# Optimization experiments

Measured on AMD Instinct MI355X. Metric: run time of the kernel, lower is better.

Reference implementation:

```python
import jax, jax.numpy as jnp
import numpy as np

EPS_D = 1e-12  # clamp for sqrt of pairwise distances (diag is exactly 0)


def tr2dist_small(Y):
    # Y: (B, k, N) -> (B, N, N); standard protein-folding coords->distance map
    k = Y.shape[1]
    Z = Y - jnp.mean(Y, axis=2, keepdims=True)
    n2 = jnp.sum(Z * Z, axis=1)                        # (B, N)
    D = n2[:, None, :] + n2[:, :, None] - 2.0 * jnp.einsum('bkn,bkm->bnm', Z, Z)
    D = 3.0 * D / k
    return jnp.sqrt(jnp.maximum(D, EPS_D))


def mean_masked(X, mask, axis, keepdims=True):
    return jnp.sum(X * mask, axis=axis, keepdims=keepdims) / jnp.sum(mask, axis=axis, keepdims=keepdims)


def get_graph_lap(X, mask):
    # X: (B, C, N), mask: (B, 1, N)
    B, C, N = X.shape
    mm = jnp.einsum('bin,bim->bnm', mask, mask)        # (B, N, N) pair mask
    X = X - mean_masked(X, mask, axis=2) * mask
    X = X / jnp.sqrt(jnp.sum(X * X, axis=2, keepdims=True) / jnp.sum(mask, axis=2, keepdims=True) + 1e-4)
    pos = 0.5 * jnp.linspace(0.0, 1.0, N)[None, :] * mask   # (B, 1, N)
    Xa = jnp.concatenate((X, pos), axis=1)
    Wd = tr2dist_small(Xa) * mm
    sigma = mean_masked(Wd, mm, axis=(1, 2))           # (B, 1, 1)
    Wd = jnp.exp(-Wd / sigma * 10.0) * mm
    Wsum = jnp.sum(Wd, axis=1)                         # (B, N)
    L = jnp.zeros_like(Wd) + Wsum[:, :, None] * jnp.eye(N, dtype=Wd.dtype)[None] - Wd
    L = 0.5 * (L + jnp.swapaxes(L, 1, 2))
    return L, Wd


def _forward(Z, mask, K0, Knet, W, Wend):
    h = 0.01
    m = mask[:, None, :]                               # (B, 1, N)
    Z = jnp.tanh(jnp.einsum('oc,bcn->bon', K0, Z)) * m
    nlayers = W.shape[0]
    for i in range(nlayers):
        L, _ = get_graph_lap(Z, m)
        Ki = Knet[i]
        Wi = W[i, :, :, :, 0]                          # (3, C, C) size-1 kernels
        cv = lambda w, x: jnp.einsum('oc,bcn->bon', w, x) * m     # conv1d, k=1
        cvT = lambda w, x: jnp.einsum('co,bcn->bon', w, x) * m    # conv_transpose1d, k=1
        mm1 = lambda x: jnp.einsum('bcn,bnm->bcm', x, L)
        Ai = Ki[0] * cv(Wi[0], Z) + mm1(Ki[1] * cv(Wi[1], Z)) + mm1(mm1(Ki[2] * cv(Wi[2], Z)))
        Ai = (Ai - mean_masked(Ai, m, axis=2)) * m
        Ai = Ai / jnp.sqrt(jnp.sum(Ai * Ai, axis=1, keepdims=True) + 0.001)
        Ai = jax.nn.relu(Ai)
        Ai = Ki[0] * cvT(Wi[0], Ai) + mm1(Ki[1] * cvT(Wi[1], Ai)) + mm1(mm1(Ki[2] * cvT(Wi[2], Ai)))
        Z = Z - h * Ai
    Zout = jnp.einsum('oc,bcn->bon', Wend[:, :, 0], Z) * m       # (B, chan_out, N)
    dists = tuple(tr2dist_small(Zout[:, 3 * i:3 * i + 3, :]) for i in range(Zout.shape[1] // 3))
    return dists + (Zout,)


def setup_inputs() -> dict:
    key = jax.random.key(0)
    ks = jax.random.split(key, 6)
    B, chan_in, chan_out, channels, N, nlayers = 16, 40, 3, 256, 1024, 6
    stdv0 = 0.1 * channels / chan_in
    return {
        'Z': jax.random.normal(ks[0], (B, chan_in, N), dtype=jnp.float32),
        'mask': jnp.ones((B, N), dtype=jnp.float32),
        'K0': jax.random.uniform(ks[1], (channels, chan_in), minval=-stdv0, maxval=stdv0, dtype=jnp.float32),
        'Knet': jax.random.uniform(ks[2], (nlayers, chan_out), minval=-stdv0, maxval=stdv0, dtype=jnp.float32),
        'W': jax.random.uniform(ks[3], (nlayers, 3, channels, channels, 1), minval=-0.1, maxval=0.1, dtype=jnp.float32),
        'Wend': 1e-4 * jax.random.normal(ks[4], (chan_out, channels, 1), dtype=jnp.float32),
    }


def reference(Z, mask, K0, Knet, W, Wend):
    return _forward(Z, mask, K0, Knet, W, Wend)
```

## Files before the change

kernel.cpp:

```cpp
#include <hip/hip_runtime.h>
#include <hip/hip_fp16.h>
#include <math.h>

#define BB 16
#define CIN 40
#define CH 256
#define NN 1024
#define KROWS 257
#define KPAD 288
#define NLAYERS 6

typedef unsigned short ush;
typedef __attribute__((ext_vector_type(8))) short bh8;
typedef __attribute__((ext_vector_type(8))) _Float16 h8;
typedef __attribute__((ext_vector_type(4))) float f4;

__device__ __forceinline__ ush bf16_rne(float x) {
  unsigned int u = __float_as_uint(x);
  u += 0x7fffu + ((u >> 16) & 1u);
  return (ush)(u >> 16);
}
__device__ __forceinline__ float bf16_f(ush h) {
  return __uint_as_float(((unsigned int)h) << 16);
}
// ... 181 lines not shown
  s1 = blockReduceSum(s1);
  s2 = blockReduceSum(s2);
  if (threadIdx.x == 0) {
    const size_t base = ((size_t)b * CH + o) * 8;
    statS1[base] = s1; statS2[base] = s2;
    #pragma unroll
    for (int k = 1; k < 8; k++) { statS1[base + k] = 0.f; statS2[base + k] = 0.f; }
  }
}

__global__ void masksum_kernel(const float* __restrict__ mask, float* __restrict__ msum,
                               float* __restrict__ pmpos) {
  const int b = blockIdx.x;
  float v = 0.f, p = 0.f;
  for (int n = threadIdx.x; n < NN; n += 256) {
    const float m = mask[b * NN + n];
    v += m;
    p += 0.5f * ((float)n * (1.0f / (NN - 1))) * m;
  }
  v = blockReduceSum(v);
  p = blockReduceSum(p);
  if (threadIdx.x == 0) { msum[b] = v; pmpos[b] = p * (1.0f / NN); }
}

__global__ void wprep_kernel(const float* __restrict__ W, ush* __restrict__ Wm,
                             ush* __restrict__ Wt) {
  __shared__ float t[64][65];
  const int mat = blockIdx.y;
  const int ty = blockIdx.x >> 2, tx = blockIdx.x & 3;
  const float* src = W + (size_t)mat * CH * CH;
  const int tid = threadIdx.x;
  const int lr = tid >> 2;
  const int lc = (tid & 3) * 16;
  float v[16];
  #pragma unroll
  for (int j = 0; j < 16; j += 4)
    *(float4*)&v[j] = *(const float4*)&src[(size_t)(ty * 64 + lr) * CH + tx * 64 + lc + j];
  ush hv[16];
  #pragma unroll
  for (int j = 0; j < 16; j++) {
    hv[j] = f2h(v[j]);
    t[lr][lc + j] = v[j];
  }
  const size_t offm = (size_t)mat * CH * CH + (size_t)(ty * 64 + lr) * CH + tx * 64 + lc;
  #pragma unroll
  for (int j = 0; j < 16; j += 4)
    *(ushort4*)&Wm[offm + j] = *(ushort4*)&hv[j];
  __syncthreads();
  #pragma unroll
  for (int j = 0; j < 16; j++) hv[j] = f2h(t[lc + j][lr]);
  const size_t offt = (size_t)mat * CH * CH + (size_t)(tx * 64 + lr) * CH + ty * 64 + lc;
  #pragma unroll
  for (int j = 0; j < 16; j += 4)
    *(ushort4*)&Wt[offt + j] = *(ushort4*)&hv[j];
}

__global__ void rowstatZ_kernel(const float* __restrict__ statS1, const float* __restrict__ statS2,
                                const float* __restrict__ msum, float* __restrict__ muZ,
                                float* __restrict__ rsZ) {
  const int b = blockIdx.x;
  const int c = threadIdx.x;
  const size_t base = ((size_t)b * CH + c) * 8;
  float S1 = 0.f, S2 = 0.f;
  #pragma unroll
  for (int k = 0; k < 8; k++) { S1 += statS1[base + k]; S2 += statS2[base + k]; }
  const float M = msum[b];
  const float mu = S1 / M;
  const float q = fmaxf(S2 - mu * S1, 0.f);
  muZ[b * CH + c] = mu;
  rsZ[b * CH + c] = 1.0f / sqrtf(q / M + 1e-4f);
}

__global__ void rowstatU_kernel(const float* __restrict__ statS1, const float* __restrict__ msum,
                                float* __restrict__ rmean) {
  const int b = blockIdx.x;
  const int c = threadIdx.x;
  const size_t base = ((size_t)b * CH + c) * 8;
  float S1 = 0.f;
  #pragma unroll
  for (int k = 0; k < 8; k++) S1 += statS1[base + k];
  rmean[b * CH + c] = S1 / msum[b];
}

__global__ void tsplitY_kernel(const float* __restrict__ Zcur, const float* __restrict__ mask,
                               const float* __restrict__ muZ, const float* __restrict__ rsZ,
                               const float* __restrict__ pmpos, ush* __restrict__ Th,
                               ush* __restrict__ Tl, float* __restrict__ n2part) {
  __shared__ float t[32][65];
  const int b = blockIdx.z;
  const int n0 = blockIdx.x * 64;
  const int k0 = blockIdx.y * 32;
  const int tid = threadIdx.x;
  const int lr = tid >> 3;
  const int lc = (tid & 7) * 8;
  const int gk = k0 + lr;
  float xv[8];
  if (gk < CH) {
    const float mu = muZ[b * CH + gk];
    const float rs = rsZ[b * CH + gk];
    const float* zr = Zcur + ((size_t)b * CH + gk) * NN + n0 + lc;
    const float* mr = mask + b * NN + n0 + lc;
    const float4 z0 = *(const float4*)&zr[0];
    const float4 z1 = *(const float4*)&zr[4];
    const float4 m0 = *(const float4*)&mr[0];
    const float4 m1 = *(const float4*)&mr[4];
    xv[0] = (z0.x - mu * m0.x) * rs; xv[1] = (z0.y - mu * m0.y) * rs;
    xv[2] = (z0.z - mu * m0.z) * rs; xv[3] = (z0.w - mu * m0.w) * rs;
    xv[4] = (z1.x - mu * m1.x) * rs; xv[5] = (z1.y - mu * m1.y) * rs;
    xv[6] = (z1.z - mu * m1.z) * rs; xv[7] = (z1.w - mu * m1.w) * rs;
  } else if (gk == CH) {
    const float pm = pmpos[b];
    #pragma unroll
    for (int j = 0; j < 8; j++) {
      const int n = n0 + lc + j;
      xv[j] = 0.5f * ((float)n * (1.0f / (NN - 1))) * mask[b * NN + n] - pm;
    }
  } else {
    #pragma unroll
    for (int j = 0; j < 8; j++) xv[j] = 0.f;
  }
  #pragma unroll
  for (int j = 0; j < 8; j++) t[lr][lc + j] = xv[j];
  __syncthreads();
  const int on = tid >> 2;
  const int ok = (tid & 3) * 8;
  ush hv[8], lv[8];
  float s = 0.f;
  #pragma unroll
  for (int j = 0; j < 8; j++) {
    const float v = t[ok + j][on];
    s += v * v;
    hv[j] = bf16_rne(v); lv[j] = bf16_rne(v - bf16_f(hv[j]));
  }
  const size_t off = ((size_t)b * NN + n0 + on) * KPAD + k0 + ok;
  *(ushort4*)&Th[off] = *(ushort4*)&hv[0];
  *(ushort4*)&Th[off + 4] = *(ushort4*)&hv[4];
  *(ushort4*)&Tl[off] = *(ushort4*)&lv[0];
  *(ushort4*)&Tl[off + 4] = *(ushort4*)&lv[4];
  s += __shfl_xor(s, 1, 64);
  s += __shfl_xor(s, 2, 64);
  if ((tid & 3) == 0) n2part[((size_t)b * 9 + blockIdx.y) * NN + n0 + on] = s;
}

__global__ void n2red_kernel(const float* __restrict__ n2part, float* __restrict__ n2) {
  const int idx = blockIdx.x * 256 + threadIdx.x;
  const int b = idx >> 10, n = idx & 1023;
  float s = 0.f;
  #pragma unroll
  for (int kb = 0; kb < 9; kb++) s += n2part[((size_t)b * 9 + kb) * NN + n];
  n2[idx] = s;
}

__global__ __launch_bounds__(256, 2)
void gram_v4_kernel(const ush* __restrict__ Yth, const ush* __restrict__ Ytl,
                    const float* __restrict__ n2, const float* __restrict__ mask,
                    ush* __restrict__ Dp, float* __restrict__ sigpart) {
  __shared__ ush lds[32768];
  const int bid = blockIdx.x;
  const int logical = (bid & 7) * 72 + (bid >> 3);
  const int b = logical / 36;
  int t = logical - b * 36;
  int ty = 0;
  while (t >= 8 - ty) { t -= 8 - ty; ++ty; }
  const int tx = ty + t;
  const int i0 = ty * 128;
  const int j0 = tx * 128;
  const ush* Ah = Yth + (size_t)b * NN * KPAD + (size_t)i0 * KPAD;
  const ush* Al = Ytl + (size_t)b * NN * KPAD + (size_t)i0 * KPAD;
  const ush* Bh = Yth + (size_t)b * NN * KPAD + (size_t)j0 * KPAD;
  const ush* Bl = Ytl + (size_t)b * NN * KPAD + (size_t)j0 * KPAD;
  f4 acc[4][4];
  const f4 z4 = {0.f, 0.f, 0.f, 0.f};
  #pragma unroll
  for (int mi = 0; mi < 4; mi++)
    #pragma unroll
    for (int ni = 0; ni < 4; ni++) acc[mi][ni] = z4;
  stageA(Ah, Al, KPAD, Bh, Bl, KPAD, 0, lds);
  __syncthreads();
  int pb = 0;
  for (int kt = 32; kt < KPAD; kt += 32) {
    stageA(Ah, Al, KPAD, Bh, Bl, KPAD, kt, lds + (pb ^ 1) * 16384);
    computeA(lds + pb * 16384, acc);
    __syncthreads();
    pb ^= 1;
  }
  computeA(lds + pb * 16384, acc);
  const int lane = threadIdx.x & 63;
  const int wid = threadIdx.x >> 6;
  const int wr = wid >> 1, wc = wid & 1;
  const int frow = lane & 15, hh = lane >> 4;
  const float scale = 3.0f / 257.0f;
  float lsum = 0.f;
  #pragma unroll
  for (int ni = 0; ni < 4; ni++) {
    const int jl = wc * 64 + ni * 16 + frow;
    const int j = j0 + jl;
    const float n2j = n2[b * NN + j];
    const float mkj = mask[b * NN + j];
    #pragma unroll
    for (int mi = 0; mi < 4; mi++) {
      const int il = wr * 64 + mi * 16 + hh * 4;
      ush dv[4];
      #pragma unroll
      for (int r = 0; r < 4; r++) {
        const int i = i0 + il + r;
        const float D = scale * (n2[b * NN + i] + n2j - 2.0f * acc[mi][ni][r]);
        const float d = sqrtf(fmaxf(D, 1e-12f));
        const float mmv = mask[b * NN + i] * mkj;
        const float wd = d * mmv;
        lsum += wd * mmv;
        dv[r] = f2h(wd);
      }
      if (ty != tx) {
        uint2 mr;
        mr.x = (unsigned)dv[0] | ((unsigned)dv[1] << 16);
        mr.y = (unsigned)dv[2] | ((unsigned)dv[3] << 16);
        *(uint2*)&Dp[((size_t)b * NN + j) * NN + i0 + il] = mr;
      }
      #pragma unroll
      for (int r = 0; r < 4; r++) {
        const unsigned v = dv[r];
        const unsigned vp = (unsigned)__shfl_xor((int)v, 1, 64);
        if ((frow & 1) == 0)
          *(unsigned*)&Dp[((size_t)b * NN + i0 + il + r) * NN + j] = v | (vp << 16);
      }
    }
  }
  if (ty != tx) lsum *= 2.0f;
  #pragma unroll
  for (int off = 32; off > 0; off >>= 1) lsum += __shfl_down(lsum, off, 64);
  __syncthreads();
  float* rbuf = (float*)lds;
  if (lane == 0) rbuf[wid] = lsum;
  __syncthreads();
  if (threadIdx.x == 0)
    sigpart[(size_t)b * 64 + ty * 8 + tx] = rbuf[0] + rbuf[1] + rbuf[2] + rbuf[3];
}

__global__ void sigfinal_kernel(const float* __restrict__ sigpart, const float* __restrict__ msum,
                                float* __restrict__ fbuf) {
  const int b = blockIdx.x;
  float v = 0.f;
  if (threadIdx.x < 64) {
    const int ty = threadIdx.x >> 3, tx = threadIdx.x & 7;
    if (ty <= tx) v = sigpart[b * 64 + threadIdx.x];
  }
  v = blockReduceSum(v);
  if (threadIdx.x == 0) { const float ms = msum[b]; fbuf[b] = -10.0f * ms * ms / v; }
}

__global__ void expw3_kernel(const ush* __restrict__ Dp, const float* __restrict__ mask,
                             const float* __restrict__ fbuf, ush* __restrict__ Wp) {
  const int b = blockIdx.y, n = blockIdx.x;
  const float fb = fbuf[b];
  const float mn = mask[b * NN + n];
  const size_t roff = ((size_t)b * NN + n) * NN;
  const int t = threadIdx.x;
  const float4 mk = ((const float4*)(mask + b * NN))[t];
  const ushort4 dp = *(const ushort4*)&Dp[roff + t * 4];
  const float w0 = expf(fb * h2f(dp.x)) * mn * mk.x;
  const float w1 = expf(fb * h2f(dp.y)) * mn * mk.y;
  const float w2 = expf(fb * h2f(dp.z)) * mn * mk.z;
  const float w3 = expf(fb * h2f(dp.w)) * mn * mk.w;
  const float s = blockReduceSum(w0 + w1 + w2 + w3);
  float v0 = -w0, v1 = -w1, v2 = -w2, v3 = -w3;
  if ((n >> 2) == t) {
    const int r = n & 3;
    if (r == 0) v0 += s; else if (r == 1) v1 += s; else if (r == 2) v2 += s; else v3 += s;
  }
  ushort4 h4;
  h4.x = f2h(v0); h4.y = f2h(v1); h4.z = f2h(v2); h4.w = f2h(v3);
  *(ushort4*)&Wp[roff + t * 4] = h4;
}

__global__ void tsplitZ_kernel(const float* __restrict__ in, ush* __restrict__ Th,
                               ush* __restrict__ Tl) {
  __shared__ float t[32][65];
  const int b = blockIdx.z;
  const int n0 = blockIdx.x * 64;
  const int k0 = blockIdx.y * 32;
  const float* src = in + (size_t)b * CH * NN;
  const int tid = threadIdx.x;
  const int lr = tid >> 3;
  const int lc = (tid & 7) * 8;
  const int gk = k0 + lr;
  *(float4*)&t[lr][lc]     = *(const float4*)&src[(size_t)gk * NN + n0 + lc];
  *(float4*)&t[lr][lc + 4] = *(const float4*)&src[(size_t)gk * NN + n0 + lc + 4];
  __syncthreads();
  const int on = tid >> 2;
  const int ok = (tid & 3) * 8;
  ush hv[8], lv[8];
  #pragma unroll
  for (int j = 0; j < 8; j++) {
    const float v = t[ok + j][on];
    hv[j] = f2h(v); lv[j] = f2h(v - h2f(hv[j]));
  }
  const size_t off = ((size_t)b * NN + n0 + on) * CH + k0 + ok;
  *(ushort4*)&Th[off] = *(ushort4*)&hv[0];
  *(ushort4*)&Th[off + 4] = *(ushort4*)&hv[4];
  *(ushort4*)&Tl[off] = *(ushort4*)&lv[0];
  *(ushort4*)&Tl[off + 4] = *(ushort4*)&lv[4];
}

__global__ __launch_bounds__(256, 2)
void cvall_kernel(const ush* __restrict__ Ap, const ush* __restrict__ Bth,
                  const ush* __restrict__ Btl, const float* __restrict__ mask,
                  const float* __restrict__ Kis, unsigned int* __restrict__ Cpack,
                  ush* __restrict__ C2h, ush* __restrict__ C2l) {
  __shared__ ush lds[32768];
  const int bid = blockIdx.x;
  const int logical = (bid & 7) * 96 + (bid >> 3);
  const int b = logical / 48;
  const int inner = logical - b * 48;
  const int c0g = inner & 7;
  const int r0g = inner >> 3;
  const int r0 = r0g * 128;
  const int c0 = c0g * 128;
  const ush* Aq = Ap + (size_t)r0 * CH;
  const ush* Bh = Bth + (size_t)b * NN * CH + (size_t)c0 * CH;
  const ush* Bl = Btl + (size_t)b * NN * CH + (size_t)c0 * CH;
  f4 acc[4][4];
  const f4 z4 = {0.f, 0.f, 0.f, 0.f};
  #pragma unroll
  for (int mi = 0; mi < 4; mi++)
    #pragma unroll
    for (int ni = 0; ni < 4; ni++) acc[mi][ni] = z4;
  stageCV(Aq, CH, Bh, Bl, CH, 0, lds);
  __syncthreads();
  int pb = 0;
  for (int kt = 32; kt < CH; kt += 32) {
    stageCV(Aq, CH, Bh, Bl, CH, kt, lds + (pb ^ 1) * 12288);
    computeCV(lds + pb * 12288, acc);
    __syncthreads();
    pb ^= 1;
  }
  computeCV(lds + pb * 12288, acc);
  __syncthreads();
  unsigned int* tl = (unsigned int*)lds;
  const int lane = threadIdx.x & 63;
  const int wid = threadIdx.x >> 6;
  const int wr = wid >> 1, wc = wid & 1;
  const int frow = lane & 15, hh = lane >> 4;
  const float alpha = Kis[r0g >> 1];
  #pragma unroll
  for (int ni = 0; ni < 4; ni++) {
    const int jl = wc * 64 + ni * 16 + frow;
    const float am = alpha * mask[b * NN + c0 + jl];
    #pragma unroll
    for (int mi = 0; mi < 4; mi++) {
      const int il = wr * 64 + mi * 16 + hh * 4;
      unsigned int pv[4];
      #pragma unroll
      for (int r = 0; r < 4; r++) {
        const float v = acc[mi][ni][r] * am;
        const ush h = f2h(v);
        const ush l = f2h(v - h2f(h));
        pv[r] = (unsigned int)h | ((unsigned int)l << 16);
      }
      const int slot = (il >> 2) ^ (jl & 31);
      *(uint4*)&tl[jl * 128 + slot * 4] = *(uint4*)pv;
    }
  }
  __syncthreads();
  const int rrow = threadIdx.x >> 1;
  const int rch = (threadIdx.x & 1) * 64;
  if (r0g < 4) {
    unsigned int* dst = Cpack + ((size_t)b * 512 + r0 + rrow) * NN + c0 + rch;
    #pragma unroll
    for (int g = 0; g < 16; g++) {
      unsigned int pw[4];
      #pragma unroll
      for (int q = 0; q < 4; q++) {
        const int jl = rch + g * 4 + q;
        const int slot = (rrow >> 2) ^ (jl & 31);
        pw[q] = tl[jl * 128 + slot * 4 + (rrow & 3)];
      }
      *(uint4*)&dst[g * 4] = *(uint4*)pw;
    }
  } else {
    const size_t obase = ((size_t)b * 256 + (r0 - 512) + rrow) * NN + c0 + rch;
    #pragma unroll
    for (int g = 0; g < 8; g++) {
      unsigned int hw[4], lw[4];
      #pragma unroll
      for (int q = 0; q < 4; q++) {
        unsigned int h2[2], l2[2];
        #pragma unroll
        for (int e = 0; e < 2; e++) {
          const int jl = rch + g * 8 + q * 2 + e;
          const int slot = (rrow >> 2) ^ (jl & 31);
          const unsigned int v = tl[jl * 128 + slot * 4 + (rrow & 3)];
          h2[e] = v & 0xffffu; l2[e] = v >> 16;
        }
        hw[q] = h2[0] | (h2[1] << 16);
        lw[q] = l2[0] | (l2[1] << 16);
      }
      *(uint4*)&C2h[obase + g * 8] = *(uint4*)hw;
      *(uint4*)&C2l[obase + g * 8] = *(uint4*)lw;
    }
  }
}

template <int OUTMODE, int STATS>
__global__ __launch_bounds__(256, 3)
void mm1_v5_kernel(const ush* __restrict__ Xh, const ush* __restrict__ Xl, const size_t xStride,
                   const ush* __restrict__ Wp,
                   const unsigned int* __restrict__ addp, const size_t aStride,
                   const float* __restrict__ zin, const float* __restrict__ mask,
                   float* __restrict__ outF, ush* __restrict__ outH, ush* __restrict__ outL,
                   float* __restrict__ statS1, float* __restrict__ statS2) {
  __shared__ ush lds[16384];
  const int bid = blockIdx.x;
  const int logical = (bid & 7) * 64 + (bid >> 3);
  const int b = logical >> 5;
  const int inner = logical & 31;
  const int n0 = (inner & 7) * 128;
  const int r0 = (inner >> 3) * 64;
  const ush* Ah = Xh + (size_t)b * xStride + (size_t)r0 * NN;
  const ush* Al = Xl + (size_t)b * xStride + (size_t)r0 * NN;
  const ush* Bp = Wp + (size_t)b * NN * NN + (size_t)n0 * NN;
  f4 acc[4][2];
  const f4 z4 = {0.f, 0.f, 0.f, 0.f};
  #pragma unroll
  for (int mi = 0; mi < 4; mi++) { acc[mi][0] = z4; acc[mi][1] = z4; }
  stageMM(Ah, Al, NN, Bp, NN, 0, lds);
  __syncthreads();
  int pb = 0;
  for (int kt = 32; kt < NN; kt += 32) {
    stageMM(Ah, Al, NN, Bp, NN, kt, lds + (pb ^ 1) * 8192);
    computeMM(lds + pb * 8192, acc);
    __syncthreads();
    pb ^= 1;
  }
  computeMM(lds + pb * 8192, acc);
  const int lane = threadIdx.x & 63;
  const int wid = threadIdx.x >> 6;
  const int frow = lane & 15, hh = lane >> 4;
  if (OUTMODE == 0) {
    __syncthreads();
    unsigned int* tl = (unsigned int*)lds;
    #pragma unroll
    for (int ni = 0; ni < 2; ni++) {
      const int jl = wid * 32 + ni * 16 + frow;
      const int col = n0 + jl;
      #pragma unroll
      for (int mi = 0; mi < 4; mi++) {
        const int il = mi * 16 + hh * 4;
        unsigned int pv[4];
        #pragma unroll
        for (int r = 0; r < 4; r++) {
          const int row = r0 + il + r;
          const unsigned int av = addp[(size_t)b * aStride + (size_t)row * NN + col];
          const float o = acc[mi][ni][r] + h2f((ush)(av & 0xffffu)) + h2f((ush)(av >> 16));
          const ush h = f2h(o);
          const ush l = f2h(o - h2f(h));
          pv[r] = (unsigned int)h | ((unsigned int)l << 16);
        }
        const int slot = (il >> 2) ^ (jl & 15);
        *(uint4*)&tl[jl * 64 + slot * 4] = *(uint4*)pv;
      }
    }
    __syncthreads();
    const int rrow = threadIdx.x >> 2;
    const int rch = (threadIdx.x & 3) * 32;
    const size_t obase = ((size_t)b * 256 + r0 + rrow) * NN + n0 + rch;
    #pragma unroll
    for (int g = 0; g < 4; g++) {
      unsigned int hw[4], lw[4];
      #pragma unroll
      for (int q = 0; q < 4; q++) {
        unsigned int h2[2], l2[2];
        #pragma unroll
        for (int e = 0; e < 2; e++) {
          const int jl = rch + g * 8 + q * 2 + e;
          const int slot = (rrow >> 2) ^ (jl & 15);
          const unsigned int v = tl[jl * 64 + slot * 4 + (rrow & 3)];
          h2[e] = v & 0xffffu; l2[e] = v >> 16;
        }
        hw[q] = h2[0] | (h2[1] << 16);
        lw[q] = l2[0] | (l2[1] << 16);
      }
      *(uint4*)&outH[obase + g * 8] = *(uint4*)hw;
      *(uint4*)&outL[obase + g * 8] = *(uint4*)lw;
    }
  } else {
    float a1[4][4];
    float a2[4][4];
    if (STATS) {
      #pragma unroll
      for (int mi = 0; mi < 4; mi++)
        #pragma unroll
        for (int r = 0; r < 4; r++) { a1[mi][r] = 0.f; a2[mi][r] = 0.f; }
    }
    #pragma unroll
    for (int ni = 0; ni < 2; ni++) {
      const int col = n0 + wid * 32 + ni * 16 + frow;
      const float mk = STATS ? mask[b * NN + col] : 0.f;
      #pragma unroll
      for (int mi = 0; mi < 4; mi++) {
        #pragma unroll
        for (int r = 0; r < 4; r++) {
          const int row = r0 + mi * 16 + hh * 4 + r;
          const unsigned int av = addp[(size_t)b * aStride + (size_t)row * NN + col];
          const float o = acc[mi][ni][r] + h2f((ush)(av & 0xffffu)) + h2f((ush)(av >> 16));
          const size_t ooff = (size_t)b * CH * NN + (size_t)row * NN + col;
          float val;
          if (OUTMODE == 1) val = o;
          else val = zin[ooff] - 0.01f * o;
          outF[ooff] = val;
          if (STATS) { a1[mi][r] += val * mk; a2[mi][r] += val * val * mk; }
        }
      }
    }
    if (STATS) {
      #pragma unroll
      for (int mi = 0; mi < 4; mi++)
        #pragma unroll
        for (int r = 0; r < 4; r++) {
          #pragma unroll
          for (int d = 1; d < 16; d <<= 1) {
            a1[mi][r] += __shfl_xor(a1[mi][r], d, 64);
            a2[mi][r] += __shfl_xor(a2[mi][r], d, 64);
          }
        }
      __syncthreads();
      float* s1b = (float*)lds;
      float* s2b = s1b + 256;
      if (frow == 0) {
        #pragma unroll
        for (int mi = 0; mi < 4; mi++)
          #pragma unroll
          for (int r = 0; r < 4; r++) {
            const int row = mi * 16 + hh * 4 + r;
            s1b[wid * 64 + row] = a1[mi][r];
            s2b[wid * 64 + row] = a2[mi][r];
          }
      }
      __syncthreads();
      if (threadIdx.x < 64) {
        const int row = threadIdx.x;
        const float p1 = s1b[row] + s1b[64 + row] + s1b[128 + row] + s1b[192 + row];
        const float p2 = s2b[row] + s2b[64 + row] + s2b[128 + row] + s2b[192 + row];
        const int nblk = n0 >> 7;
        statS1[((size_t)b * CH + r0 + row) * 8 + nblk] = p1;
        statS2[((size_t)b * CH + r0 + row) * 8 + nblk] = p2;
      }
    }
  }
}

__global__ void csq_kernel(const float* __restrict__ U, const float* __restrict__ mask,
                           const float* __restrict__ rmean, float* __restrict__ part) {
  const int b = blockIdx.y, cc = blockIdx.x;
  const int n = threadIdx.x * 4;
  const float4 m4 = *(const float4*)&mask[b * NN + n];
  float4 s4 = {0.f, 0.f, 0.f, 0.f};
  for (int r = 0; r < 16; r++) {
    const int c = cc * 16 + r;
    const float rm = rmean[b * CH + c];
    const float4 u4 = *(const float4*)&U[((size_t)b * CH + c) * NN + n];
    float a;
    a = (u4.x - rm) * m4.x; s4.x += a * a;
    a = (u4.y - rm) * m4.y; s4.y += a * a;
    a = (u4.z - rm) * m4.z; s4.z += a * a;
    a = (u4.w - rm) * m4.w; s4.w += a * a;
  }
  *(float4*)&part[((size_t)(b * 16 + cc)) * NN + n] = s4;
}

__global__ void csq2_kernel(const float* __restrict__ part, float* __restrict__ rs) {
  const int b = blockIdx.y;
  const int n = blockIdx.x * 256 + threadIdx.x;
  float s = 0.001f;
  #pragma unroll
  for (int cc = 0; cc < 16; cc++) s += part[((size_t)(b * 16 + cc)) * NN + n];
  rs[b * NN + n] = 1.0f / sqrtf(s);
}

__global__ void tsplitN_kernel(const float* __restrict__ U, const float* __restrict__ mask,
                               const float* __restrict__ rmean, const float* __restrict__ rs,
                               ush* __restrict__ Th, ush* __restrict__ Tl) {
  __shared__ float t[32][65];
  const int b = blockIdx.z;
  const int n0 = blockIdx.x * 64;
  const int k0 = blockIdx.y * 32;
  const int tid = threadIdx.x;
  const int lr = tid >> 3;
  const int lc = (tid & 7) * 8;
  const int gc = k0 + lr;
  const float rm = rmean[b * CH + gc];
  const float4 ma = *(const float4*)&mask[b * NN + n0 + lc];
  const float4 mb = *(const float4*)&mask[b * NN + n0 + lc + 4];
  const float4 ra = *(const float4*)&rs[b * NN + n0 + lc];
  const float4 rb = *(const float4*)&rs[b * NN + n0 + lc + 4];
  const float4 ua = *(const float4*)&U[((size_t)b * CH + gc) * NN + n0 + lc];
  const float4 ub = *(const float4*)&U[((size_t)b * CH + gc) * NN + n0 + lc + 4];
  t[lr][lc + 0] = fmaxf((ua.x - rm) * ma.x * ra.x, 0.f);
  t[lr][lc + 1] = fmaxf((ua.y - rm) * ma.y * ra.y, 0.f);
  t[lr][lc + 2] = fmaxf((ua.z - rm) * ma.z * ra.z, 0.f);
  t[lr][lc + 3] = fmaxf((ua.w - rm) * ma.w * ra.w, 0.f);
  t[lr][lc + 4] = fmaxf((ub.x - rm) * mb.x * rb.x, 0.f);
  t[lr][lc + 5] = fmaxf((ub.y - rm) * mb.y * rb.y, 0.f);
  t[lr][lc + 6] = fmaxf((ub.z - rm) * mb.z * rb.z, 0.f);
  t[lr][lc + 7] = fmaxf((ub.w - rm) * mb.w * rb.w, 0.f);
  __syncthreads();
  const int on = tid >> 2;
  const int ok = (tid & 3) * 8;
  ush hv[8], lv[8];
  #pragma unroll
  for (int j = 0; j < 8; j++) {
    const float v = t[ok + j][on];
    hv[j] = f2h(v); lv[j] = f2h(v - h2f(hv[j]));
  }
  const size_t off = ((size_t)b * NN + n0 + on) * CH + k0 + ok;
  *(ushort4*)&Th[off] = *(ushort4*)&hv[0];
  *(ushort4*)&Th[off + 4] = *(ushort4*)&hv[4];
  *(ushort4*)&Tl[off] = *(ushort4*)&lv[0];
  *(ushort4*)&Tl[off + 4] = *(ushort4*)&lv[4];
}

__global__ void zout_kernel(const float* __restrict__ Z, const float* __restrict__ Wend,
                            const float* __restrict__ mask, float* __restrict__ outZ,
                            float* __restrict__ Zcent) {
  const int b = blockIdx.x;
  __shared__ float w[3 * CH];
  for (int i = threadIdx.x; i < 3 * CH; i += 256) w[i] = Wend[i];
  __syncthreads();
  float a[3][4];
  #pragma unroll
  for (int j = 0; j < 4; j++) { a[0][j] = 0.f; a[1][j] = 0.f; a[2][j] = 0.f; }
  const float* Zb = Z + (size_t)b * CH * NN;
  for (int c = 0; c < CH; c++) {
    const float w0 = w[c], w1 = w[CH + c], w2 = w[2 * CH + c];
    #pragma unroll
    for (int j = 0; j < 4; j++) {
      float zv = Zb[(size_t)c * NN + threadIdx.x + j * 256];
      a[0][j] += w0 * zv; a[1][j] += w1 * zv; a[2][j] += w2 * zv;
    }
  }
  float sum[3] = {0.f, 0.f, 0.f};
  #pragma unroll
  for (int j = 0; j < 4; j++) {
    const int n = threadIdx.x + j * 256;
    const float mv = mask[b * NN + n];
    #pragma unroll
    for (int o = 0; o < 3; o++) {
      a[o][j] *= mv;
      outZ[((size_t)b * 3 + o) * NN + n] = a[o][j];
      sum[o] += a[o][j];
    }
  }
  for (int o = 0; o < 3; o++) {
    float s = blockReduceSum(sum[o]);
    const float mean = s * (1.0f / NN);
    #pragma unroll
    for (int j = 0; j < 4; j++) {
      const int n = threadIdx.x + j * 256;
      Zcent[((size_t)b * 3 + o) * NN + n] = a[o][j] - mean;
    }
  }
}

__global__ void dist_kernel(const float* __restrict__ Zcent, float* __restrict__ outD) {
  const int b = blockIdx.z;
  const int n = blockIdx.y;
  const int m = blockIdx.x * 256 + threadIdx.x;
  const float* Zb = Zcent + (size_t)b * 3 * NN;
  const float x0 = Zb[n], x1 = Zb[NN + n], x2 = Zb[2 * NN + n];
  const float d0 = x0 - Zb[m], d1 = x1 - Zb[NN + m], d2 = x2 - Zb[2 * NN + m];
  const float D = d0 * d0 + d1 * d1 + d2 * d2;
  outD[((size_t)b * NN + n) * NN + m] = sqrtf(fmaxf(D, 1e-12f));
}

extern "C" void kernel_launch(void* const* d_in, const int* in_sizes, int n_in,
                              void* d_out, int out_size, void* d_ws, size_t ws_size,
                              hipStream_t stream) {
  const float* Zin  = (const float*)d_in[0];
  const float* mask = (const float*)d_in[1];
  const float* K0   = (const float*)d_in[2];
  const float* Knet = (const float*)d_in[3];
  const float* W    = (const float*)d_in[4];
  const float* Wend = (const float*)d_in[5];
  float* out = (float*)d_out;

  ush* Wp = (ush*)out;
  ush* Dp = Wp + (size_t)BB * NN * NN;
  float* outZ = out + (size_t)BB * NN * NN;

  float* p = (float*)d_ws;
  float* uni = p; p += (size_t)BB * 768 * NN;
  ush* Yth = (ush*)uni;
  ush* Ytl = Yth + (size_t)BB * NN * KPAD;
  unsigned int* Cpack = (unsigned int*)uni;
  ush* C2h = (ush*)(uni + (size_t)BB * 512 * NN);
  ush* C2l = C2h + (size_t)BB * 256 * NN;

  float* Zcur = p; p += (size_t)BB * CH * NN;
  float* U    = p; p += (size_t)BB * CH * NN;
  ush* Zth = (ush*)p; p += (size_t)BB * NN * CH / 2;
  ush* Ztl = (ush*)p; p += (size_t)BB * NN * CH / 2;
  ush* Thb = Zth;
  ush* Tlb = Ztl;
  ush* Wm = (ush*)p; p += (size_t)18 * CH * CH / 2;
  ush* Wt = (ush*)p; p += (size_t)18 * CH * CH / 2;
  float* n2b   = p; p += BB * NN;
  float* rsb   = p; p += BB * NN;
  float* msum  = p; p += BB;
  float* pmpos = p; p += BB;
  float* sigp  = p; p += BB * 64;
  float* fbuf  = p; p += BB;
  float* rmeanb= p; p += BB * CH;
  float* muZ   = p; p += BB * CH;
  float* rsZ   = p; p += BB * CH;
  float* statS1= p; p += (size_t)BB * CH * 8;
  float* statS2= p; p += (size_t)BB * CH * 8;
  float* n2part= p; p += (size_t)BB * 9 * NN;
  float* partb = p; p += (size_t)BB * 16 * NN;
  float* Zcent = p; p += BB * 3 * NN;

  const dim3 gtsZ(NN / 64, CH / 32, BB);
  const dim3 gtsY(NN / 64, KPAD / 32, BB);
  const size_t sC = (size_t)512 * NN;
  const size_t sT = (size_t)CH * NN;

  masksum_kernel<<<BB, 256, 0, stream>>>(mask, msum, pmpos);
  wprep_kernel<<<dim3(16, 18), 256, 0, stream>>>(W, Wm, Wt);
  k0_kernel<<<dim3(CH, BB), 256, 0, stream>>>(Zin, K0, mask, Zcur, statS1, statS2);

  for (int layer = 0; layer < NLAYERS; layer++) {
    rowstatZ_kernel<<<BB, 256, 0, stream>>>(statS1, statS2, msum, muZ, rsZ);
    tsplitY_kernel<<<gtsY, 256, 0, stream>>>(Zcur, mask, muZ, rsZ, pmpos, Yth, Ytl, n2part);
    n2red_kernel<<<BB * NN / 256, 256, 0, stream>>>(n2part, n2b);
    gram_v4_kernel<<<576, 256, 0, stream>>>(Yth, Ytl, n2b, mask, Dp, sigp);
    sigfinal_kernel<<<BB, 256, 0, stream>>>(sigp, msum, fbuf);
    expw3_kernel<<<dim3(NN, BB), 256, 0, stream>>>(Dp, mask, fbuf, Wp);
    tsplitZ_kernel<<<gtsZ, 256, 0, stream>>>(Zcur, Zth, Ztl);

    const ush* Am = Wm + (size_t)layer * 3 * CH * CH;
    const ush* At = Wt + (size_t)layer * 3 * CH * CH;
    const float* Ki = Knet + layer * 3;

    cvall_kernel<<<768, 256, 0, stream>>>(Am, Zth, Ztl, mask, Ki, Cpack, C2h, C2l);
    mm1_v5_kernel<0, 0><<<512, 256, 0, stream>>>(C2h, C2l, sT, Wp,
        Cpack + (size_t)256 * NN, sC, nullptr, nullptr, nullptr, Thb, Tlb, nullptr, nullptr);
    mm1_v5_kernel<1, 1><<<512, 256, 0, stream>>>(Thb, Tlb, sT, Wp,
        Cpack, sC, nullptr, mask, U, nullptr, nullptr, statS1, statS2);

    rowstatU_kernel<<<BB, 256, 0, stream>>>(statS1, msum, rmeanb);
    csq_kernel<<<dim3(16, BB), 256, 0, stream>>>(U, mask, rmeanb, partb);
    csq2_kernel<<<dim3(NN / 256, BB), 256, 0, stream>>>(partb, rsb);
    tsplitN_kernel<<<gtsZ, 256, 0, stream>>>(U, mask, rmeanb, rsb, Zth, Ztl);

    cvall_kernel<<<768, 256, 0, stream>>>(At, Zth, Ztl, mask, Ki, Cpack, C2h, C2l);
    mm1_v5_kernel<0, 0><<<512, 256, 0, stream>>>(C2h, C2l, sT, Wp,
        Cpack + (size_t)256 * NN, sC, nullptr, nullptr, nullptr, Thb, Tlb, nullptr, nullptr);
    mm1_v5_kernel<2, 1><<<512, 256, 0, stream>>>(Thb, Tlb, sT, Wp,
        Cpack, sC, Zcur, mask, Zcur, nullptr, nullptr, statS1, statS2);
  }

  zout_kernel<<<BB, 256, 0, stream>>>(Zcur, Wend, mask, outZ, Zcent);
  dist_kernel<<<dim3(NN / 256, NN, BB), 256, 0, stream>>>(Zcent, out);
}
```

Measured before the change: 1.801 ms.

## Emit fp16 hi/lo split Z and U from mm1 epilogue, drop separate transposes

```diff
diff --git a/kernel.cpp b/kernel.cpp
--- a/kernel.cpp
+++ b/kernel.cpp
@@ -287,64 +287,89 @@
   rmean[b * CH + c] = S1 / msum[b];
 }
 
-__global__ void tsplitY_kernel(const float* __restrict__ Zcur, const float* __restrict__ mask,
-                               const float* __restrict__ muZ, const float* __restrict__ rsZ,
-                               const float* __restrict__ pmpos, ush* __restrict__ Th,
-                               ush* __restrict__ Tl, float* __restrict__ n2part) {
+__global__ void tsplitZ_kernel(const float* __restrict__ in, ush* __restrict__ Th,
+                               ush* __restrict__ Tl) {
   __shared__ float t[32][65];
   const int b = blockIdx.z;
   const int n0 = blockIdx.x * 64;
   const int k0 = blockIdx.y * 32;
+  const float* src = in + (size_t)b * CH * NN;
   const int tid = threadIdx.x;
   const int lr = tid >> 3;
   const int lc = (tid & 7) * 8;
   const int gk = k0 + lr;
-  float xv[8];
-  if (gk < CH) {
-    const float mu = muZ[b * CH + gk];
-    const float rs = rsZ[b * CH + gk];
-    const float* zr = Zcur + ((size_t)b * CH + gk) * NN + n0 + lc;
-    const float* mr = mask + b * NN + n0 + lc;
-    const float4 z0 = *(const float4*)&zr[0];
-    const float4 z1 = *(const float4*)&zr[4];
-    const float4 m0 = *(const float4*)&mr[0];
-    const float4 m1 = *(const float4*)&mr[4];
-    xv[0] = (z0.x - mu * m0.x) * rs; xv[1] = (z0.y - mu * m0.y) * rs;
-    xv[2] = (z0.z - mu * m0.z) * rs; xv[3] = (z0.w - mu * m0.w) * rs;
-    xv[4] = (z1.x - mu * m1.x) * rs; xv[5] = (z1.y - mu * m1.y) * rs;
-    xv[6] = (z1.z - mu * m1.z) * rs; xv[7] = (z1.w - mu * m1.w) * rs;
-  } else if (gk == CH) {
-    const float pm = pmpos[b];
-    #pragma unroll
-    for (int j = 0; j < 8; j++) {
-      const int n = n0 + lc + j;
-      xv[j] = 0.5f * ((float)n * (1.0f / (NN - 1))) * mask[b * NN + n] - pm;
-    }
-  } else {
-    #pragma unroll
-    for (int j = 0; j < 8; j++) xv[j] = 0.f;
-  }
-  #pragma unroll
-  for (int j = 0; j < 8; j++) t[lr][lc + j] = xv[j];
+  *(float4*)&t[lr][lc]     = *(const float4*)&src[(size_t)gk * NN + n0 + lc];
+  *(float4*)&t[lr][lc + 4] = *(const float4*)&src[(size_t)gk * NN + n0 + lc + 4];
   __syncthreads();
   const int on = tid >> 2;
   const int ok = (tid & 3) * 8;
   ush hv[8], lv[8];
-  float s = 0.f;
   #pragma unroll
   for (int j = 0; j < 8; j++) {
     const float v = t[ok + j][on];
-    s += v * v;
-    hv[j] = bf16_rne(v); lv[j] = bf16_rne(v - bf16_f(hv[j]));
-  }
-  const size_t off = ((size_t)b * NN + n0 + on) * KPAD + k0 + ok;
+    hv[j] = f2h(v); lv[j] = f2h(v - h2f(hv[j]));
+  }
+  const size_t off = ((size_t)b * NN + n0 + on) * CH + k0 + ok;
+  *(ushort4*)&Th[off] = *(ushort4*)&hv[0];
+  *(ushort4*)&Th[off + 4] = *(ushort4*)&hv[4];
+  *(ushort4*)&Tl[off] = *(ushort4*)&lv[0];
+  *(ushort4*)&Tl[off + 4] = *(ushort4*)&lv[4];
+}
+
+__global__ void tsplitY2_kernel(const ush* __restrict__ Zsh, const ush* __restrict__ Zsl,
+                                const float* __restrict__ mask, const float* __restrict__ muZ,
+                                const float* __restrict__ rsZ, const float* __restrict__ pmpos,
+                                ush* __restrict__ Th, ush* __restrict__ Tl,
+                                float* __restrict__ n2part) {
+  const int b = blockIdx.z;
+  const int n0 = blockIdx.x * 64;
+  const int k0 = blockIdx.y * 32;
+  const int tid = threadIdx.x;
+  const int n = n0 + (tid >> 2);
+  const int kc = k0 + (tid & 3) * 8;
+  const float mn = mask[b * NN + n];
+  float val[8];
+  if (kc + 7 < CH) {
+    const size_t zoff = ((size_t)b * NN + n) * CH + kc;
+    const ushort4 h0 = *(const ushort4*)&Zsh[zoff];
+    const ushort4 h1 = *(const ushort4*)&Zsh[zoff + 4];
+    const ushort4 l0 = *(const ushort4*)&Zsl[zoff];
+    const ushort4 l1 = *(const ushort4*)&Zsl[zoff + 4];
+    const float4 mu0 = *(const float4*)&muZ[b * CH + kc];
+    const float4 mu1 = *(const float4*)&muZ[b * CH + kc + 4];
+    const float4 rs0 = *(const float4*)&rsZ[b * CH + kc];
+    const float4 rs1 = *(const float4*)&rsZ[b * CH + kc + 4];
+    val[0] = (h2f(h0.x) + h2f(l0.x) - mu0.x * mn) * rs0.x;
+    val[1] = (h2f(h0.y) + h2f(l0.y) - mu0.y * mn) * rs0.y;
+    val[2] = (h2f(h0.z) + h2f(l0.z) - mu0.z * mn) * rs0.z;
+    val[3] = (h2f(h0.w) + h2f(l0.w) - mu0.w * mn) * rs0.w;
+    val[4] = (h2f(h1.x) + h2f(l1.x) - mu1.x * mn) * rs1.x;
+    val[5] = (h2f(h1.y) + h2f(l1.y) - mu1.y * mn) * rs1.y;
+    val[6] = (h2f(h1.z) + h2f(l1.z) - mu1.z * mn) * rs1.z;
+    val[7] = (h2f(h1.w) + h2f(l1.w) - mu1.w * mn) * rs1.w;
+  } else {
+    #pragma unroll
+    for (int j = 0; j < 8; j++) {
+      const int gk = kc + j;
+      val[j] = (gk == CH) ? (0.5f * ((float)n * (1.0f / (NN - 1))) * mn - pmpos[b]) : 0.f;
+    }
+  }
+  float s = 0.f;
+  ush hv[8], lv[8];
+  #pragma unroll
+  for (int j = 0; j < 8; j++) {
+    s += val[j] * val[j];
+    hv[j] = bf16_rne(val[j]);
+    lv[j] = bf16_rne(val[j] - bf16_f(hv[j]));
+  }
+  const size_t off = ((size_t)b * NN + n) * KPAD + kc;
   *(ushort4*)&Th[off] = *(ushort4*)&hv[0];
   *(ushort4*)&Th[off + 4] = *(ushort4*)&hv[4];
   *(ushort4*)&Tl[off] = *(ushort4*)&lv[0];
   *(ushort4*)&Tl[off + 4] = *(ushort4*)&lv[4];
   s += __shfl_xor(s, 1, 64);
   s += __shfl_xor(s, 2, 64);
-  if ((tid & 3) == 0) n2part[((size_t)b * 9 + blockIdx.y) * NN + n0 + on] = s;
+  if ((tid & 3) == 0) n2part[((size_t)b * 9 + blockIdx.y) * NN + n] = s;
 }
 
 __global__ void n2red_kernel(const float* __restrict__ n2part, float* __restrict__ n2) {
@@ -478,35 +503,6 @@
   *(ushort4*)&Wp[roff + t * 4] = h4;
 }
 
-__global__ void tsplitZ_kernel(const float* __restrict__ in, ush* __restrict__ Th,
-                               ush* __restrict__ Tl) {
-  __shared__ float t[32][65];
-  const int b = blockIdx.z;
-  const int n0 = blockIdx.x * 64;
-  const int k0 = blockIdx.y * 32;
-  const float* src = in + (size_t)b * CH * NN;
-  const int tid = threadIdx.x;
-  const int lr = tid >> 3;
-  const int lc = (tid & 7) * 8;
-  const int gk = k0 + lr;
-  *(float4*)&t[lr][lc]     = *(const float4*)&src[(size_t)gk * NN + n0 + lc];
-  *(float4*)&t[lr][lc + 4] = *(const float4*)&src[(size_t)gk * NN + n0 + lc + 4];
-  __syncthreads();
-  const int on = tid >> 2;
-  const int ok = (tid & 3) * 8;
-  ush hv[8], lv[8];
-  #pragma unroll
-  for (int j = 0; j < 8; j++) {
-    const float v = t[ok + j][on];
-    hv[j] = f2h(v); lv[j] = f2h(v - h2f(hv[j]));
-  }
-  const size_t off = ((size_t)b * NN + n0 + on) * CH + k0 + ok;
-  *(ushort4*)&Th[off] = *(ushort4*)&hv[0];
-  *(ushort4*)&Th[off + 4] = *(ushort4*)&hv[4];
-  *(ushort4*)&Tl[off] = *(ushort4*)&lv[0];
-  *(ushort4*)&Tl[off + 4] = *(ushort4*)&lv[4];
-}
-
 __global__ __launch_bounds__(256, 2)
 void cvall_kernel(const ush* __restrict__ Ap, const ush* __restrict__ Bth,
                   const ush* __restrict__ Btl, const float* __restrict__ mask,
@@ -608,7 +604,7 @@
 
 template <int OUTMODE, int STATS>
 __global__ __launch_bounds__(256, 3)
-void mm1_v5_kernel(const ush* __restrict__ Xh, const ush* __restrict__ Xl, const size_t xStride,
+void mm1_v6_kernel(const ush* __restrict__ Xh, const ush* __restrict__ Xl, const size_t xStride,
                    const ush* __restrict__ Wp,
                    const unsigned int* __restrict__ addp, const size_t aStride,
                    const float* __restrict__ zin, const float* __restrict__ mask,
@@ -641,31 +637,49 @@
   const int lane = threadIdx.x & 63;
   const int wid = threadIdx.x >> 6;
   const int frow = lane & 15, hh = lane >> 4;
+  float a1[4][4];
+  float a2[4][4];
+  if (STATS) {
+    #pragma unroll
+    for (int mi = 0; mi < 4; mi++)
+      #pragma unroll
+      for (int r = 0; r < 4; r++) { a1[mi][r] = 0.f; a2[mi][r] = 0.f; }
+  }
+  __syncthreads();
+  unsigned int* tl = (unsigned int*)lds;
+  #pragma unroll
+  for (int ni = 0; ni < 2; ni++) {
+    const int jl = wid * 32 + ni * 16 + frow;
+    const int col = n0 + jl;
+    const float mk = STATS ? mask[b * NN + col] : 0.f;
+    #pragma unroll
+    for (int mi = 0; mi < 4; mi++) {
+      const int il = mi * 16 + hh * 4;
+      unsigned int pv[4];
+      #pragma unroll
+      for (int r = 0; r < 4; r++) {
+        const int row = r0 + il + r;
+        const unsigned int av = addp[(size_t)b * aStride + (size_t)row * NN + col];
+        const float o = acc[mi][ni][r] + h2f((ush)(av & 0xffffu)) + h2f((ush)(av >> 16));
+        float val;
+        if (OUTMODE == 2) {
+          const size_t ooff = (size_t)b * CH * NN + (size_t)row * NN + col;
+          val = zin[ooff] - 0.01f * o;
+          outF[ooff] = val;
+        } else {
+          val = o;
+        }
+        if (STATS) { a1[mi][r] += val * mk; a2[mi][r] += val * val * mk; }
+        const ush h = f2h(val);
+        const ush l = f2h(val - h2f(h));
+        pv[r] = (unsigned int)h | ((unsigned int)l << 16);
+      }
+      const int slot = (il >> 2) ^ (jl & 15);
+      *(uint4*)&tl[jl * 64 + slot * 4] = *(uint4*)pv;
+    }
+  }
+  __syncthreads();
   if (OUTMODE == 0) {
-    __syncthreads();
-    unsigned int* tl = (unsigned int*)lds;
-    #pragma unroll
-    for (int ni = 0; ni < 2; ni++) {
-      const int jl = wid * 32 + ni * 16 + frow;
-      const int col = n0 + jl;
-      #pragma unroll
-      for (int mi = 0; mi < 4; mi++) {
-        const int il = mi * 16 + hh * 4;
-        unsigned int pv[4];
-        #pragma unroll
-        for (int r = 0; r < 4; r++) {
-          const int row = r0 + il + r;
-          const unsigned int av = addp[(size_t)b * aStride + (size_t)row * NN + col];
-          const float o = acc[mi][ni][r] + h2f((ush)(av & 0xffffu)) + h2f((ush)(av >> 16));
-          const ush h = f2h(o);
-          const ush l = f2h(o - h2f(h));
-          pv[r] = (unsigned int)h | ((unsigned int)l << 16);
-        }
-        const int slot = (il >> 2) ^ (jl & 15);
-        *(uint4*)&tl[jl * 64 + slot * 4] = *(uint4*)pv;
-      }
-    }
-    __syncthreads();
     const int rrow = threadIdx.x >> 2;
     const int rch = (threadIdx.x & 3) * 32;
     const size_t obase = ((size_t)b * 256 + r0 + rrow) * NN + n0 + rch;
@@ -689,73 +703,66 @@
       *(uint4*)&outL[obase + g * 8] = *(uint4*)lw;
     }
   } else {
-    float a1[4][4];
-    float a2[4][4];
-    if (STATS) {
-      #pragma unroll
-      for (int mi = 0; mi < 4; mi++)
+    const int nloc = threadIdx.x >> 1;
+    const int ch0 = (threadIdx.x & 1) * 32;
+    #pragma unroll
+    for (int half = 0; half < 2; half++) {
+      unsigned int hw[8], lw[8];
+      #pragma unroll
+      for (int q = 0; q < 8; q++) {
+        const int ila = ch0 + half * 16 + q * 2;
+        const int ilb = ila + 1;
+        const unsigned int va = tl[nloc * 64 + (((ila >> 2) ^ (nloc & 15)) << 2) + (ila & 3)];
+        const unsigned int vb = tl[nloc * 64 + (((ilb >> 2) ^ (nloc & 15)) << 2) + (ilb & 3)];
+        hw[q] = (va & 0xffffu) | (vb << 16);
+        lw[q] = (va >> 16) | (vb & 0xffff0000u);
+      }
+      const size_t zoff = ((size_t)b * NN + n0 + nloc) * CH + r0 + ch0 + half * 16;
+      *(uint4*)&outH[zoff] = *(uint4*)&hw[0];
+      *(uint4*)&outH[zoff + 8] = *(uint4*)&hw[4];
+      *(uint4*)&outL[zoff] = *(uint4*)&lw[0];
+      *(uint4*)&outL[zoff + 8] = *(uint4*)&lw[4];
+    }
+  }
+  if (STATS) {
+    #pragma unroll
+    for (int mi = 0; mi < 4; mi++)
+      #pragma unroll
+      for (int r = 0; r < 4; r++) {
         #pragma unroll
-        for (int r = 0; r < 4; r++) { a1[mi][r] = 0.f; a2[mi][r] = 0.f; }
-    }
-    #pragma unroll
-    for (int ni = 0; ni < 2; ni++) {
-      const int col = n0 + wid * 32 + ni * 16 + frow;
-      const float mk = STATS ? mask[b * NN + col] : 0.f;
-      #pragma unroll
-      for (int mi = 0; mi < 4; mi++) {
-        #pragma unroll
-        for (int r = 0; r < 4; r++) {
-          const int row = r0 + mi * 16 + hh * 4 + r;
-          const unsigned int av = addp[(size_t)b * aStride + (size_t)row * NN + col];
-          const float o = acc[mi][ni][r] + h2f((ush)(av & 0xffffu)) + h2f((ush)(av >> 16));
-          const size_t ooff = (size_t)b * CH * NN + (size_t)row * NN + col;
-          float val;
-          if (OUTMODE == 1) val = o;
-          else val = zin[ooff] - 0.01f * o;
-          outF[ooff] = val;
-          if (STATS) { a1[mi][r] += val * mk; a2[mi][r] += val * val * mk; }
+        for (int d = 1; d < 16; d <<= 1) {
+          a1[mi][r] += __shfl_xor(a1[mi][r], d, 64);
+          a2[mi][r] += __shfl_xor(a2[mi][r], d, 64);
         }
       }
-    }
-    if (STATS) {
+    __syncthreads();
+    float* s1b = (float*)lds;
+    float* s2b = s1b + 256;
+    if (frow == 0) {
       #pragma unroll
       for (int mi = 0; mi < 4; mi++)
         #pragma unroll
         for (int r = 0; r < 4; r++) {
-          #pragma unroll
-          for (int d = 1; d < 16; d <<= 1) {
-            a1[mi][r] += __shfl_xor(a1[mi][r], d, 64);
-            a2[mi][r] += __shfl_xor(a2[mi][r], d, 64);
-          }
+          const int row = mi * 16 + hh * 4 + r;
+          s1b[wid * 64 + row] = a1[mi][r];
+          s2b[wid * 64 + row] = a2[mi][r];
         }
-      __syncthreads();
-      float* s1b = (float*)lds;
-      float* s2b = s1b + 256;
-      if (frow == 0) {
-        #pragma unroll
-        for (int mi = 0; mi < 4; mi++)
-          #pragma unroll
-          for (int r = 0; r < 4; r++) {
-            const int row = mi * 16 + hh * 4 + r;
-            s1b[wid * 64 + row] = a1[mi][r];
-            s2b[wid * 64 + row] = a2[mi][r];
-          }
-      }
-      __syncthreads();
-      if (threadIdx.x < 64) {
-        const int row = threadIdx.x;
-        const float p1 = s1b[row] + s1b[64 + row] + s1b[128 + row] + s1b[192 + row];
-        const float p2 = s2b[row] + s2b[64 + row] + s2b[128 + row] + s2b[192 + row];
-        const int nblk = n0 >> 7;
-        statS1[((size_t)b * CH + r0 + row) * 8 + nblk] = p1;
-        statS2[((size_t)b * CH + r0 + row) * 8 + nblk] = p2;
-      }
-    }
-  }
-}
-
-__global__ void csq_kernel(const float* __restrict__ U, const float* __restrict__ mask,
-                           const float* __restrict__ rmean, float* __restrict__ part) {
+    }
+    __syncthreads();
+    if (threadIdx.x < 64) {
+      const int row = threadIdx.x;
+      const float p1 = s1b[row] + s1b[64 + row] + s1b[128 + row] + s1b[192 + row];
+      const float p2 = s2b[row] + s2b[64 + row] + s2b[128 + row] + s2b[192 + row];
+      const int nblk = n0 >> 7;
+      statS1[((size_t)b * CH + r0 + row) * 8 + nblk] = p1;
+      statS2[((size_t)b * CH + r0 + row) * 8 + nblk] = p2;
+    }
+  }
+}
+
+__global__ void csq_kernel(const ush* __restrict__ Uh, const ush* __restrict__ Ul,
+                           const float* __restrict__ mask, const float* __restrict__ rmean,
+                           float* __restrict__ part) {
   const int b = blockIdx.y, cc = blockIdx.x;
   const int n = threadIdx.x * 4;
   const float4 m4 = *(const float4*)&mask[b * NN + n];
@@ -763,12 +770,14 @@
   for (int r = 0; r < 16; r++) {
     const int c = cc * 16 + r;
     const float rm = rmean[b * CH + c];
-    const float4 u4 = *(const float4*)&U[((size_t)b * CH + c) * NN + n];
+    const size_t uoff = ((size_t)b * 256 + c) * NN + n;
+    const ushort4 uh = *(const ushort4*)&Uh[uoff];
+    const ushort4 ul = *(const ushort4*)&Ul[uoff];
     float a;
-    a = (u4.x - rm) * m4.x; s4.x += a * a;
-    a = (u4.y - rm) * m4.y; s4.y += a * a;
-    a = (u4.z - rm) * m4.z; s4.z += a * a;
-    a = (u4.w - rm) * m4.w; s4.w += a * a;
+    a = (h2f(uh.x) + h2f(ul.x) - rm) * m4.x; s4.x += a * a;
+    a = (h2f(uh.y) + h2f(ul.y) - rm) * m4.y; s4.y += a * a;
+    a = (h2f(uh.z) + h2f(ul.z) - rm) * m4.z; s4.z += a * a;
+    a = (h2f(uh.w) + h2f(ul.w) - rm) * m4.w; s4.w += a * a;
   }
   *(float4*)&part[((size_t)(b * 16 + cc)) * NN + n] = s4;
 }
@@ -782,9 +791,10 @@
   rs[b * NN + n] = 1.0f / sqrtf(s);
 }
 
-__global__ void tsplitN_kernel(const float* __restrict__ U, const float* __restrict__ mask,
-                               const float* __restrict__ rmean, const float* __restrict__ rs,
-                               ush* __restrict__ Th, ush* __restrict__ Tl) {
+__global__ void tsplitN2_kernel(const ush* __restrict__ Uh, const ush* __restrict__ Ul,
+                                const float* __restrict__ mask, const float* __restrict__ rmean,
+                                const float* __restrict__ rs, ush* __restrict__ Th,
+                                ush* __restrict__ Tl) {
   __shared__ float t[32][65];
   const int b = blockIdx.z;
   const int n0 = blockIdx.x * 64;
@@ -798,16 +808,19 @@
   const float4 mb = *(const float4*)&mask[b * NN + n0 + lc + 4];
   const float4 ra = *(const float4*)&rs[b * NN + n0 + lc];
   const float4 rb = *(const float4*)&rs[b * NN + n0 + lc + 4];
-  const float4 ua = *(const float4*)&U[((size_t)b * CH + gc) * NN + n0 + lc];
-  const float4 ub = *(const float4*)&U[((size_t)b * CH + gc) * NN + n0 + lc + 4];
-  t[lr][lc + 0] = fmaxf((ua.x - rm) * ma.x * ra.x, 0.f);
-  t[lr][lc + 1] = fmaxf((ua.y - rm) * ma.y * ra.y, 0.f);
-  t[lr][lc + 2] = fmaxf((ua.z - rm) * ma.z * ra.z, 0.f);
-  t[lr][lc + 3] = fmaxf((ua.w - rm) * ma.w * ra.w, 0.f);
-  t[lr][lc + 4] = fmaxf((ub.x - rm) * mb.x * rb.x, 0.f);
-  t[lr][lc + 5] = fmaxf((ub.y - rm) * mb.y * rb.y, 0.f);
-  t[lr][lc + 6] = fmaxf((ub.z - rm) * mb.z * rb.z, 0.f);
-  t[lr][lc + 7] = fmaxf((ub.w - rm) * mb.w * rb.w, 0.f);
+  const size_t uoff = ((size_t)b * 256 + gc) * NN + n0 + lc;
+  const ushort4 ha = *(const ushort4*)&Uh[uoff];
+  const ushort4 hb = *(const ushort4*)&Uh[uoff + 4];
+  const ushort4 la = *(const ushort4*)&Ul[uoff];
+  const ushort4 lb = *(const ushort4*)&Ul[uoff + 4];
+  t[lr][lc + 0] = fmaxf((h2f(ha.x) + h2f(la.x) - rm) * ma.x * ra.x, 0.f);
+  t[lr][lc + 1] = fmaxf((h2f(ha.y) + h2f(la.y) - rm) * ma.y * ra.y, 0.f);
+  t[lr][lc + 2] = fmaxf((h2f(ha.z) + h2f(la.z) - rm) * ma.z * ra.z, 0.f);
+  t[lr][lc + 3] = fmaxf((h2f(ha.w) + h2f(la.w) - rm) * ma.w * ra.w, 0.f);
+  t[lr][lc + 4] = fmaxf((h2f(hb.x) + h2f(lb.x) - rm) * mb.x * rb.x, 0.f);
+  t[lr][lc + 5] = fmaxf((h2f(hb.y) + h2f(lb.y) - rm) * mb.y * rb.y, 0.f);
+  t[lr][lc + 6] = fmaxf((h2f(hb.z) + h2f(lb.z) - rm) * mb.z * rb.z, 0.f);
+  t[lr][lc + 7] = fmaxf((h2f(hb.w) + h2f(lb.w) - rm) * mb.w * rb.w, 0.f);
   __syncthreads();
   const int on = tid >> 2;
   const int ok = (tid & 3) * 8;
@@ -901,11 +914,10 @@
   ush* C2l = C2h + (size_t)BB * 256 * NN;
 
   float* Zcur = p; p += (size_t)BB * CH * NN;
-  float* U    = p; p += (size_t)BB * CH * NN;
-  ush* Zth = (ush*)p; p += (size_t)BB * NN * CH / 2;
-  ush* Ztl = (ush*)p; p += (size_t)BB * NN * CH / 2;
-  ush* Thb = Zth;
-  ush* Tlb = Ztl;
+  ush* Thb = (ush*)p; p += (size_t)BB * NN * CH / 2;
+  ush* Tlb = (ush*)p; p += (size_t)BB * NN * CH / 2;
+  ush* Zsh = (ush*)p; p += (size_t)BB * NN * CH / 2;
+  ush* Zsl = (ush*)p; p += (size_t)BB * NN * CH / 2;
   ush* Wm = (ush*)p; p += (size_t)18 * CH * CH / 2;
   ush* Wt = (ush*)p; p += (size_t)18 * CH * CH / 2;
   float* n2b   = p; p += BB * NN;
@@ -931,36 +943,36 @@
   masksum_kernel<<<BB, 256, 0, stream>>>(mask, msum, pmpos);
   wprep_kernel<<<dim3(16, 18), 256, 0, stream>>>(W, Wm, Wt);
   k0_kernel<<<dim3(CH, BB), 256, 0, stream>>>(Zin, K0, mask, Zcur, statS1, statS2);
+  tsplitZ_kernel<<<gtsZ, 256, 0, stream>>>(Zcur, Zsh, Zsl);
 
   for (int layer = 0; layer < NLAYERS; layer++) {
     rowstatZ_kernel<<<BB, 256, 0, stream>>>(statS1, statS2, msum, muZ, rsZ);
-    tsplitY_kernel<<<gtsY, 256, 0, stream>>>(Zcur, mask, muZ, rsZ, pmpos, Yth, Ytl, n2part);
+    tsplitY2_kernel<<<gtsY, 256, 0, stream>>>(Zsh, Zsl, mask, muZ, rsZ, pmpos, Yth, Ytl, n2part);
     n2red_kernel<<<BB * NN / 256, 256, 0, stream>>>(n2part, n2b);
     gram_v4_kernel<<<576, 256, 0, stream>>>(Yth, Ytl, n2b, mask, Dp, sigp);
     sigfinal_kernel<<<BB, 256, 0, stream>>>(sigp, msum, fbuf);
     expw3_kernel<<<dim3(NN, BB), 256, 0, stream>>>(Dp, mask, fbuf, Wp);
-    tsplitZ_kernel<<<gtsZ, 256, 0, stream>>>(Zcur, Zth, Ztl);
 
     const ush* Am = Wm + (size_t)layer * 3 * CH * CH;
     const ush* At = Wt + (size_t)layer * 3 * CH * CH;
     const float* Ki = Knet + layer * 3;
 
-    cvall_kernel<<<768, 256, 0, stream>>>(Am, Zth, Ztl, mask, Ki, Cpack, C2h, C2l);
-    mm1_v5_kernel<0, 0><<<512, 256, 0, stream>>>(C2h, C2l, sT, Wp,
+    cvall_kernel<<<768, 256, 0, stream>>>(Am, Zsh, Zsl, mask, Ki, Cpack, C2h, C2l);
+    mm1_v6_kernel<0, 0><<<512, 256, 0, stream>>>(C2h, C2l, sT, Wp,
         Cpack + (size_t)256 * NN, sC, nullptr, nullptr, nullptr, Thb, Tlb, nullptr, nullptr);
-    mm1_v5_kernel<1, 1><<<512, 256, 0, stream>>>(Thb, Tlb, sT, Wp,
-        Cpack, sC, nullptr, mask, U, nullptr, nullptr, statS1, statS2);
+    mm1_v6_kernel<0, 1><<<512, 256, 0, stream>>>(Thb, Tlb, sT, Wp,
+        Cpack, sC, nullptr, mask, nullptr, C2h, C2l, statS1, statS2);
 
     rowstatU_kernel<<<BB, 256, 0, stream>>>(statS1, msum, rmeanb);
-    csq_kernel<<<dim3(16, BB), 256, 0, stream>>>(U, mask, rmeanb, partb);
+    csq_kernel<<<dim3(16, BB), 256, 0, stream>>>(C2h, C2l, mask, rmeanb, partb);
     csq2_kernel<<<dim3(NN / 256, BB), 256, 0, stream>>>(partb, rsb);
-    tsplitN_kernel<<<gtsZ, 256, 0, stream>>>(U, mask, rmeanb, rsb, Zth, Ztl);
-
-    cvall_kernel<<<768, 256, 0, stream>>>(At, Zth, Ztl, mask, Ki, Cpack, C2h, C2l);
-    mm1_v5_kernel<0, 0><<<512, 256, 0, stream>>>(C2h, C2l, sT, Wp,
+    tsplitN2_kernel<<<gtsZ, 256, 0, stream>>>(C2h, C2l, mask, rmeanb, rsb, Thb, Tlb);
+
+    cvall_kernel<<<768, 256, 0, stream>>>(At, Thb, Tlb, mask, Ki, Cpack, C2h, C2l);
+    mm1_v6_kernel<0, 0><<<512, 256, 0, stream>>>(C2h, C2l, sT, Wp,
         Cpack + (size_t)256 * NN, sC, nullptr, nullptr, nullptr, Thb, Tlb, nullptr, nullptr);
-    mm1_v5_kernel<2, 1><<<512, 256, 0, stream>>>(Thb, Tlb, sT, Wp,
-        Cpack, sC, Zcur, mask, Zcur, nullptr, nullptr, statS1, statS2);
+    mm1_v6_kernel<2, 1><<<512, 256, 0, stream>>>(Thb, Tlb, sT, Wp,
+        Cpack, sC, Zcur, mask, Zcur, Zsh, Zsl, statS1, statS2);
   }
 
   zout_kernel<<<BB, 256, 0, stream>>>(Zcur, Wend, mask, outZ, Zcent);
```

Result: no change. 1.806 ms (+0.3%).
